# Kernel optimization log

Measured on AMD Instinct MI355X. Metric: run time of the kernel, lower is better.

## Reference

```python
import jax, jax.numpy as jnp
import numpy as np

B, L, IN, DM, DS, DC, EXP = 4, 1024, 256, 1024, 16, 4, 2
DI = EXP * DM            # d_inner = 2048
DTR = (DM + 15) // 16    # dt_rank = 64


def setup_inputs() -> dict:
    key = jax.random.key(0)
    ks = jax.random.split(key, 10)
    s = lambda k, sh, sc: jax.random.normal(k, sh, jnp.float32) * sc
    return {
        "x": s(ks[0], (B, L, IN), 1.0),
        "W_emb": s(ks[1], (DM, IN), IN ** -0.5),
        "b_emb": jnp.zeros((DM,), jnp.float32),
        "in_proj_w": s(ks[2], (2 * DI, DM), DM ** -0.5),
        "conv_w": s(ks[3], (DI, 1, DC), DC ** -0.5),
        "conv_b": jnp.zeros((DI,), jnp.float32),
        "x_proj_w": s(ks[4], (DTR + 2 * DS, DI), DI ** -0.5),
        "dt_proj_w": s(ks[5], (DI, DTR), DTR ** -0.5),
        "dt_proj_b": s(ks[6], (DI,), 0.1),
        "A_log": jnp.tile(jnp.log(jnp.arange(1, DS + 1, dtype=jnp.float32)), (DI, 1)),
        "D": jnp.ones((DI,), jnp.float32),
        "out_proj_w": s(ks[7], (DM, DI), DI ** -0.5),
        "fc_w": s(ks[8], (1, DM), DM ** -0.5),
        "fc_b": jnp.zeros((1,), jnp.float32),
    }


def _forward(x, W_emb, b_emb, in_proj_w, conv_w, conv_b, x_proj_w,
             dt_proj_w, dt_proj_b, A_log, D, out_proj_w, fc_w, fc_b):
    h = x @ W_emb.T + b_emb                      # [B,L,DM] input embedding
    xz = h @ in_proj_w.T                         # [B,L,2*DI]
    u, z = jnp.split(xz, 2, axis=-1)             # each [B,L,DI]
    # causal depthwise conv over time (pad left d_conv-1)
    uc = jax.lax.conv_general_dilated(
        u.transpose(0, 2, 1), conv_w, (1,), [(DC - 1, 0)],
        dimension_numbers=('NCH', 'OIH', 'NCH'), feature_group_count=DI)
    u = jax.nn.silu(uc.transpose(0, 2, 1) + conv_b)   # [B,L,DI]
    xdbl = u @ x_proj_w.T                        # [B,L,DTR+2*DS]
    dt, Bm, Cm = jnp.split(xdbl, [DTR, DTR + DS], axis=-1)
    delta = jax.nn.softplus(dt @ dt_proj_w.T + dt_proj_b)  # [B,L,DI]
    A = -jnp.exp(A_log)                          # [DI,DS]

    def step(hst, ins):
        d_t, B_t, C_t, u_t = ins                 # [B,DI],[B,DS],[B,DS],[B,DI]
        dA = jnp.exp(d_t[..., None] * A)         # [B,DI,DS]
        hst = dA * hst + (d_t * u_t)[..., None] * B_t[:, None, :]
        y = jnp.einsum('bds,bs->bd', hst, C_t)
        return hst, y

    h0 = jnp.zeros((B, DI, DS), u.dtype)
    _, ys = jax.lax.scan(step, h0, (delta.transpose(1, 0, 2),
                                    Bm.transpose(1, 0, 2),
                                    Cm.transpose(1, 0, 2),
                                    u.transpose(1, 0, 2)))
    y = ys.transpose(1, 0, 2) + D * u            # [B,L,DI] with D skip
    y = y * jax.nn.silu(z)                       # gate
    out = y @ out_proj_w.T                       # [B,L,DM]
    return out[:, -1, :] @ fc_w.T + fc_b         # [B,1]


def reference(x, W_emb, b_emb, in_proj_w, conv_w, conv_b, x_proj_w,
              dt_proj_w, dt_proj_b, A_log, D, out_proj_w, fc_w, fc_b):
    return _forward(x, W_emb, b_emb, in_proj_w, conv_w, conv_b, x_proj_w,
                    dt_proj_w, dt_proj_b, A_log, D, out_proj_w, fc_w, fc_b)
```

## Files before the change

### kernel.cpp

```cpp
#include <hip/hip_runtime.h>
#include <cstddef>
#include <cstdint>

namespace {

typedef _Float16 half8 __attribute__((ext_vector_type(8)));
typedef _Float16 half4 __attribute__((ext_vector_type(4)));
typedef float f32x4 __attribute__((ext_vector_type(4)));

constexpr int Bn   = 4;
constexpr int Ln   = 1024;
constexpr int INn  = 256;
constexpr int DMn  = 1024;
constexpr int DSn  = 16;
constexpr int DCn  = 4;
constexpr int DIn  = 2048;
constexpr int DTRn = 64;
constexpr int XPW  = DTRn + DSn;
constexpr int NCHUNK = 64;
constexpr int CHUNK  = Ln / NCHUNK;
constexpr int WCH  = 32;
constexpr int ML   = Bn * Ln;

__device__ __forceinline__ float silu_(float x) { return x / (1.f + __expf(-x)); }
__device__ __forceinline__ float softplus_(float x) {
    return fmaxf(x, 0.f) + __logf(1.f + __expf(-fabsf(x)));
}

__global__ __launch_bounds__(256)
void prep_mega(const float* __restrict__ x, _Float16* __restrict__ xh,
               const float* __restrict__ ip, _Float16* __restrict__ iph,
               const float* __restrict__ dtw, _Float16* __restrict__ dtwh,
               const float* __restrict__ W_emb, _Float16* __restrict__ W_embT,
               const float* __restrict__ x_proj, _Float16* __restrict__ xp_h,
               const float* __restrict__ fc_w, const float* __restrict__ out_w,
               float* __restrict__ wp,
               const float* __restrict__ b_emb, float* __restrict__ badd,
               const float* __restrict__ fc_b, float* __restrict__ out) {
    __shared__ float tile[32][33];
    const int bid = blockIdx.x, tid = threadIdx.x;
    if (bid < 4096) {
        const int n = bid;
        const float4 v = ((const float4*)ip)[n * 256 + tid];
        ((half4*)iph)[n * 256 + tid] =
            half4{(_Float16)v.x, (_Float16)v.y, (_Float16)v.z, (_Float16)v.w};
        const float4 bv = ((const float4*)b_emb)[tid];
        float s = v.x * bv.x + v.y * bv.y + v.z * bv.z + v.w * bv.w;
        for (int off = 32; off > 0; off >>= 1) s += __shfl_down(s, off);
        if ((tid & 63) == 0) tile[0][tid >> 6] = s;
        __syncthreads();
        if (tid == 0) badd[n] = tile[0][0] + tile[0][1] + tile[0][2] + tile[0][3];
    } else if (bid < 5248) {
        const float* in; _Float16* outp; int i;
        if (bid < 5120) { in = x;   outp = xh;   i = (bid - 4096) * 256 + tid; }
        else            { in = dtw; outp = dtwh; i = (bid - 5120) * 256 + tid; }
        const float4 v = ((const float4*)in)[i];
        ((half4*)outp)[i] = half4{(_Float16)v.x, (_Float16)v.y, (_Float16)v.z, (_Float16)v.w};
    } else if (bid < 5504) {
        const int bx = bid - 5248;
        const int m0 = (bx & 31) * 32, c0 = (bx >> 5) * 32;
        const int lc = tid & 31, lr = tid >> 5;
        #pragma unroll
        for (int ph = 0; ph < 4; ++ph)
            tile[lr + ph * 8][lc] = W_emb[(size_t)(m0 + lr + ph * 8) * INn + c0 + lc];
        __syncthreads();
        #pragma unroll
        for (int ph = 0; ph < 4; ++ph)
            W_embT[(size_t)(c0 + lr + ph * 8) * DMn + m0 + lc] = (_Float16)tile[lc][lr + ph * 8];
    } else if (bid < 5760) {
        const int i = (bid - 5504) * 256 + tid;
        const int r = i >> 9;
        const int c4 = i & 511;
        half4 h;
        if (r < XPW) {
            const float4 v = ((const float4*)(x_proj + (size_t)r * DIn))[c4];
            h = half4{(_Float16)v.x, (_Float16)v.y, (_Float16)v.z, (_Float16)v.w};
        } else {
            h = half4{(_Float16)0.f, (_Float16)0.f, (_Float16)0.f, (_Float16)0.f};
        }
        ((half4*)(xp_h + (size_t)r * DIn))[c4] = h;
    } else if (bid < 6016) {
        const int bx = bid - 5760;
        const int d = (bx & 7) * 256 + tid;
        const int c = bx >> 3;
        const int mstep = DMn / WCH;
        float s = 0.f;
        for (int m = c * mstep; m < (c + 1) * mstep; ++m)
            s += fc_w[m] * out_w[(size_t)m * DIn + d];
        wp[(size_t)c * DIn + d] = s;
    } else {
        if (tid < Bn) out[tid] = fc_b[0];
    }
}

__global__ __launch_bounds__(256)
void skgemm2(const _Float16* __restrict__ A, int lda,
             const _Float16* __restrict__ Bw, int ldb,
             float* __restrict__ P, int N, int Kc) {
    __shared__ _Float16 As[128 * 32];
    __shared__ _Float16 Bs[128 * 32];
    const int tid  = threadIdx.x;
    const int lane = tid & 63, wid = tid >> 6;
    const int wm = wid >> 1, wn = wid & 1;
    const int sk = blockIdx.x;
    const int m0 = blockIdx.y * 128;
    const int n0 = blockIdx.z * 128;
    const int M  = gridDim.y * 128;

    f32x4 acc[4][4] = {};
    const int kbeg = sk * Kc;
    for (int k0 = kbeg; k0 < kbeg + Kc; k0 += 32) {
        #pragma unroll
        for (int i = 0; i < 2; ++i) {
            const int off = tid * 16 + i * 4096;
            const int row = off >> 6;
            const int ch  = (off & 63) >> 1;
            const _Float16* ga = A  + (size_t)(m0 + row) * lda + k0 + ch;
            const _Float16* gb = Bw + (size_t)(n0 + row) * ldb + k0 + ch;
            __builtin_amdgcn_global_load_lds(
                (const __attribute__((address_space(1))) void*)ga,
                (__attribute__((address_space(3))) void*)(&As[off >> 1]), 16, 0, 0);
            __builtin_amdgcn_global_load_lds(
                (const __attribute__((address_space(1))) void*)gb,
                (__attribute__((address_space(3))) void*)(&Bs[off >> 1]), 16, 0, 0);
        }
        __syncthreads();
        const int ar = lane & 15;
        const int kq = (lane >> 4) * 8;
        half8 af[4], bf[4];
        #pragma unroll
        for (int i = 0; i < 4; ++i)
            af[i] = *(const half8*)&As[(wm * 64 + i * 16 + ar) * 32 + kq];
        #pragma unroll
        for (int j = 0; j < 4; ++j)
            bf[j] = *(const half8*)&Bs[(wn * 64 + j * 16 + ar) * 32 + kq];
        #pragma unroll
        for (int i = 0; i < 4; ++i)
            #pragma unroll
            for (int j = 0; j < 4; ++j)
                acc[i][j] = __builtin_amdgcn_mfma_f32_16x16x32_f16(af[i], bf[j], acc[i][j], 0, 0, 0);
        __syncthreads();
    }

    const int cr = (lane >> 4) * 4;
    const int cn = lane & 15;
    #pragma unroll
    for (int i = 0; i < 4; ++i) {
        #pragma unroll
        for (int j = 0; j < 4; ++j) {
            const int n = n0 + wn * 64 + j * 16 + cn;
            if (n < N) {
                #pragma unroll
                for (int r = 0; r < 4; ++r) {
                    const int m = m0 + wm * 64 + i * 16 + cr + r;
                    P[((size_t)sk * M + m) * N + n] = acc[i][j][r];
                }
            }
        }
    }
}

__global__ __launch_bounds__(256)
void skcomb(const float* __restrict__ P, _Float16* __restrict__ out, int total, int nsk) {
    const int i = blockIdx.x * 256 + threadIdx.x;
    if (i >= total) return;
    float s = 0.f;
    for (int k = 0; k < nsk; ++k) s += P[(size_t)k * total + i];
    out[i] = (_Float16)s;
}

__global__ __launch_bounds__(256)
void skcombB_clast(const float* __restrict__ P, _Float16* __restrict__ dtBh,
                   const _Float16* __restrict__ u, const float* __restrict__ x_proj,
                   float* __restrict__ Clast) {
    const int bid = blockIdx.x, tid = threadIdx.x;
    if (bid < 1280) {
        const int i = bid * 256 + tid;
        float s = 0.f;
        #pragma unroll
        for (int k = 0; k < 8; ++k) s += P[(size_t)k * (ML * XPW) + i];
        dtBh[i] = (_Float16)s;
    } else {
        const int wave = tid >> 6, lane = tid & 63;
        const int task = (bid - 1280) * 4 + wave;
        const int s_idx = task & 15, b = task >> 4;
        const _Float16* ur = u + ((size_t)b * Ln + (Ln - 1)) * DIn;
        const float* w = x_proj + (size_t)(XPW + s_idx) * DIn;
        float s = 0.f;
        for (int k = lane; k < DIn; k += 64) s += (float)ur[k] * w[k];
        for (int off = 32; off > 0; off >>= 1) s += __shfl_down(s, off);
        if (lane == 0) Clast[b * DSn + s_idx] = s;
    }
}

template<int ACT, bool HAS_BIAS>
__global__ __launch_bounds__(256)
void hgemm(const _Float16* __restrict__ A, int lda,
           const _Float16* __restrict__ Bw, int ldb,
           const float* __restrict__ bias,
           _Float16* __restrict__ Ch, int ldc,
           int N, int K) {
    __shared__ _Float16 As[128 * 32];
    __shared__ _Float16 Bs[128 * 32];
    const int tid  = threadIdx.x;
    const int lane = tid & 63, wid = tid >> 6;
    const int wm = wid >> 1, wn = wid & 1;
    const int m0 = blockIdx.y * 128, n0 = blockIdx.x * 128;

    f32x4 acc[4][4] = {};

    for (int k0 = 0; k0 < K; k0 += 32) {
        #pragma unroll
        for (int i = 0; i < 2; ++i) {
            const int off = tid * 16 + i * 4096;
            const int row = off >> 6;
            const int ch  = (off & 63) >> 1;
            const _Float16* ga = A  + (size_t)(m0 + row) * lda + k0 + ch;
            const _Float16* gb = Bw + (size_t)(n0 + row) * ldb + k0 + ch;
            __builtin_amdgcn_global_load_lds(
                (const __attribute__((address_space(1))) void*)ga,
                (__attribute__((address_space(3))) void*)(&As[off >> 1]), 16, 0, 0);
            __builtin_amdgcn_global_load_lds(
                (const __attribute__((address_space(1))) void*)gb,
                (__attribute__((address_space(3))) void*)(&Bs[off >> 1]), 16, 0, 0);
        }
        __syncthreads();

        const int ar = lane & 15;
        const int kq = (lane >> 4) * 8;
        half8 af[4], bf[4];
        #pragma unroll
        for (int i = 0; i < 4; ++i)
            af[i] = *(const half8*)&As[(wm * 64 + i * 16 + ar) * 32 + kq];
        #pragma unroll
        for (int j = 0; j < 4; ++j)
            bf[j] = *(const half8*)&Bs[(wn * 64 + j * 16 + ar) * 32 + kq];
        #pragma unroll
        for (int i = 0; i < 4; ++i)
            #pragma unroll
            for (int j = 0; j < 4; ++j)
                acc[i][j] = __builtin_amdgcn_mfma_f32_16x16x32_f16(af[i], bf[j], acc[i][j], 0, 0, 0);
        __syncthreads();
    }

    const int cr = (lane >> 4) * 4;
    const int cn = lane & 15;
    #pragma unroll
    for (int i = 0; i < 4; ++i) {
        #pragma unroll
        for (int j = 0; j < 4; ++j) {
            const int n = n0 + wn * 64 + j * 16 + cn;
            if (n < N) {
                #pragma unroll
                for (int r = 0; r < 4; ++r) {
                    const int m = m0 + wm * 64 + i * 16 + cr + r;
                    float v = acc[i][j][r];
                    if (HAS_BIAS) v += bias[n];
                    if (ACT == 1) v = softplus_(v);
                    Ch[(size_t)m * ldc + n] = (_Float16)v;
                }
            }
        }
    }
}

__global__ __launch_bounds__(256)
void conv_zlast(const _Float16* __restrict__ upre, const float* __restrict__ cw,
                const float* __restrict__ cb, _Float16* __restrict__ uh,
                const float* __restrict__ x, const _Float16* __restrict__ Wfh,
                const float* __restrict__ badd, float* __restrict__ zlast) {
    const int tid = threadIdx.x;
    const int bid = blockIdx.x;
    if (bid < 1024) {
        const int b  = bid >> 8;
        const int t0 = (bid & 255) * 4;
        const int d0 = tid * 8;
        const size_t rowbase = ((size_t)b * Ln + t0) * DIn + d0;

        half8 hzero;
        #pragma unroll
        for (int q = 0; q < 8; ++q) hzero[q] = (_Float16)0.f;

        half8 rows[7];
        if (t0 >= 3) {
            #pragma unroll
            for (int r = 0; r < 7; ++r)
                rows[r] = *(const half8*)(upre + rowbase + (ptrdiff_t)(r - 3) * DIn);
        } else {
            #pragma unroll
            for (int r = 0; r < 7; ++r) {
                const int t = t0 - 3 + r;
                rows[r] = (t >= 0) ? *(const half8*)(upre + rowbase + (ptrdiff_t)(r - 3) * DIn) : hzero;
            }
        }

        f32x4 cwq[8];
        float cbv[8];
        #pragma unroll
        for (int q = 0; q < 8; ++q) {
            cwq[q] = *(const f32x4*)(cw + (size_t)(d0 + q) * DCn);
            cbv[q] = cb[d0 + q];
        }

        #pragma unroll
        for (int s = 0; s < 4; ++s) {
            half8 o;
            #pragma unroll
            for (int q = 0; q < 8; ++q) {
                float acc = cbv[q];
                #pragma unroll
                for (int j = 0; j < DCn; ++j) acc += (float)rows[s + j][q] * cwq[q][j];
                o[q] = (_Float16)silu_(acc);
            }
            *(half8*)(uh + rowbase + (size_t)s * DIn) = o;
        }
    } else {
        const int task = (bid - 1024) * 256 + tid;
        const int j = task & (DIn - 1), b = task >> 11;
        const float4* x4 = (const float4*)(x + ((size_t)b * Ln + (Ln - 1)) * INn);
        const half4* w4 = (const half4*)(Wfh + (size_t)(DIn + j) * INn);
        float s = 0.f;
        #pragma unroll 8
        for (int q = 0; q < 64; ++q) {
            const float4 xv = x4[q];
            const half4 wv = w4[q];
            s += (float)wv[0] * xv.x + (float)wv[1] * xv.y
               + (float)wv[2] * xv.z + (float)wv[3] * xv.w;
        }
        zlast[(size_t)b * DIn + j] = s + badd[DIn + j];
    }
}

__global__ __launch_bounds__(256)
void scan_chunk_kernel(const _Float16* __restrict__ delta, const _Float16* __restrict__ u,
                       const _Float16* __restrict__ dtBh, const float* __restrict__ A_log,
                       float* __restrict__ cS, _Float16* __restrict__ cH) {
    const int d = blockIdx.x * 256 + threadIdx.x;
    const int c = blockIdx.y, b = blockIdx.z;
    float A[DSn], h[DSn];
    const float4* al = (const float4*)(A_log + (size_t)d * DSn);
    #pragma unroll
    for (int q = 0; q < 4; ++q) {
        const float4 v = al[q];
        A[q * 4 + 0] = -__expf(v.x); A[q * 4 + 1] = -__expf(v.y);
        A[q * 4 + 2] = -__expf(v.z); A[q * 4 + 3] = -__expf(v.w);
        h[q * 4 + 0] = 0.f; h[q * 4 + 1] = 0.f; h[q * 4 + 2] = 0.f; h[q * 4 + 3] = 0.f;
    }
    const float A0 = A[0];
    bool structured = true;
    #pragma unroll
    for (int s = 1; s < DSn; ++s)
        structured = structured && (fabsf(A[s] - (float)(s + 1) * A0) <= 1e-4f * (s + 1));

    float Ssum = 0.f;
    const size_t base = ((size_t)b * Ln + (size_t)c * CHUNK) * DIn + d;
    const _Float16* Bp = dtBh + ((size_t)b * Ln + (size_t)c * CHUNK) * XPW + DTRn;
    if (structured) {
        #pragma unroll 4
        for (int tt = 0; tt < CHUNK; ++tt) {
            const float dl = (float)delta[base + (size_t)tt * DIn];
            const float uu = (float)u[base + (size_t)tt * DIn];
            const float du = dl * uu;
            Ssum += dl;
            const half8 bv0 = *(const half8*)(Bp + tt * XPW);
            const half8 bv1 = *(const half8*)(Bp + tt * XPW + 8);
            float Bv[DSn];
            #pragma unroll
            for (int q = 0; q < 8; ++q) { Bv[q] = (float)bv0[q]; Bv[8 + q] = (float)bv1[q]; }
            const float e1 = __expf(dl * A0);
            const float e2 = e1 * e1, e4 = e2 * e2, e8 = e4 * e4;
            float E[DSn];
            E[0] = e1;      E[1] = e2;      E[2] = e2 * e1;  E[3] = e4;
            E[4] = e4 * e1; E[5] = e4 * e2; E[6] = E[5] * e1; E[7] = e8;
            E[8] = e8 * e1; E[9] = e8 * e2; E[10] = E[9] * e1; E[11] = e8 * e4;
            E[12] = E[11] * e1; E[13] = E[11] * e2; E[14] = E[13] * e1; E[15] = e8 * e8;
            #pragma unroll
            for (int s = 0; s < DSn; ++s) h[s] = E[s] * h[s] + du * Bv[s];
        }
    } else {
        #pragma unroll 4
        for (int tt = 0; tt < CHUNK; ++tt) {
            const float dl = (float)delta[base + (size_t)tt * DIn];
            const float uu = (float)u[base + (size_t)tt * DIn];
            const float du = dl * uu;
            Ssum += dl;
            const half8 bv0 = *(const half8*)(Bp + tt * XPW);
            const half8 bv1 = *(const half8*)(Bp + tt * XPW + 8);
            float Bv[DSn];
            #pragma unroll
            for (int q = 0; q < 8; ++q) { Bv[q] = (float)bv0[q]; Bv[8 + q] = (float)bv1[q]; }
            #pragma unroll
            for (int s = 0; s < DSn; ++s) h[s] = __expf(dl * A[s]) * h[s] + du * Bv[s];
        }
    }
    const size_t cidx = ((size_t)b * NCHUNK + c) * DIn + d;
    cS[cidx] = Ssum;
    half8 o0, o1;
    #pragma unroll
    for (int q = 0; q < 8; ++q) { o0[q] = (_Float16)h[q]; o1[q] = (_Float16)h[8 + q]; }
    *(half8*)(cH + cidx * DSn) = o0;
    *(half8*)(cH + cidx * DSn + 8) = o1;
}

__global__ __launch_bounds__(256)
void combine_v3(const float* __restrict__ cS, const _Float16* __restrict__ cH,
                const float* __restrict__ A_log, const float* __restrict__ Clast,
                const float* __restrict__ Dp, const _Float16* __restrict__ u,
                const float* __restrict__ zlast, const float* __restrict__ wp,
                float* __restrict__ out) {
    __shared__ float acc[16];
    const int tid = threadIdx.x;
    const int s = tid & 15;
    const int d = blockIdx.x * 16 + (tid >> 4);
    const int b = blockIdx.y;
    const float A = -__expf(A_log[(size_t)d * DSn + s]);
    float h = 0.f;
    const size_t cb0 = (size_t)b * NCHUNK;
    for (int c = 0; c < NCHUNK; ++c) {
        const size_t cidx = (cb0 + c) * DIn + d;
        h = __expf(A * cS[cidx]) * h + (float)cH[cidx * DSn + s];
    }
    float y = h * Clast[b * DSn + s];
    y += __shfl_xor(y, 1);
    y += __shfl_xor(y, 2);
    y += __shfl_xor(y, 4);
    y += __shfl_xor(y, 8);
    if (s == 0) {
        const float ul = (float)u[((size_t)b * Ln + (Ln - 1)) * DIn + d];
        float yy = y + Dp[d] * ul;
        yy *= silu_(zlast[(size_t)b * DIn + d]);
        float w = 0.f;
        #pragma unroll
        for (int c = 0; c < WCH; ++c) w += wp[(size_t)c * DIn + d];
        acc[tid >> 4] = yy * w;
    }
    __syncthreads();
    if (tid == 0) {
        float t = 0.f;
        #pragma unroll
        for (int i = 0; i < 16; ++i) t += acc[i];
        atomicAdd(&out[b], t);
    }
}

}

extern "C" void kernel_launch(void* const* d_in, const int* in_sizes, int n_in,
                              void* d_out, int out_size, void* d_ws, size_t ws_size,
                              hipStream_t stream) {
    (void)in_sizes; (void)n_in; (void)out_size; (void)ws_size;
    const float* x       = (const float*)d_in[0];
    const float* W_emb   = (const float*)d_in[1];
    const float* b_emb   = (const float*)d_in[2];
    const float* in_proj = (const float*)d_in[3];
    const float* conv_w  = (const float*)d_in[4];
    const float* conv_b  = (const float*)d_in[5];
    const float* x_proj  = (const float*)d_in[6];
    const float* dt_w    = (const float*)d_in[7];
    const float* dt_b    = (const float*)d_in[8];
    const float* A_log   = (const float*)d_in[9];
    const float* Dp      = (const float*)d_in[10];
    const float* out_w   = (const float*)d_in[11];
    const float* fc_w    = (const float*)d_in[12];
    const float* fc_b    = (const float*)d_in[13];
    float* out = (float*)d_out;
    char* w8 = (char*)d_ws;

    const size_t MB = 1ull << 20;
    _Float16* upreh    = (_Float16*)(w8);
    _Float16* uh       = (_Float16*)(w8 + 16 * MB);
    float*    wfoldP   = (float*)(w8 + 32 * MB);
    _Float16* deltah   = (_Float16*)(w8 + 32 * MB);
    float*    skp      = (float*)(w8 + 48 * MB);
    float*    cS       = skp;
    _Float16* cH       = (_Float16*)(w8 + 50 * MB);
    _Float16* dtBh     = (_Float16*)(w8 + 67 * MB);
    _Float16* xh       = (_Float16*)(w8 + 68 * MB);
    _Float16* W_embT_h = (_Float16*)(w8 + 70 * MB);
    _Float16* in_projh = (_Float16*)(w8 + 71 * MB);
    _Float16* xp_h     = (_Float16*)(w8 + 79 * MB);
    _Float16* dt_wh    = (_Float16*)(w8 + 80 * MB);
    _Float16* Wfoldh   = (_Float16*)(w8 + 81 * MB);
    float*    wp       = (float*)(w8 + 83 * MB);
    float*    badd     = (float*)(w8 + 84 * MB);
    float*    zlast    = badd + 4096;
    float*    Clast    = zlast + (size_t)Bn * DIn;

    prep_mega<<<6017, 256, 0, stream>>>(x, xh, in_proj, in_projh, dt_w, dt_wh,
                                        W_emb, W_embT_h, x_proj, xp_h,
                                        fc_w, out_w, wp, b_emb, badd, fc_b, out);

    skgemm2<<<dim3(4, ML / 128, 2), 256, 0, stream>>>(
        in_projh, DMn, W_embT_h, DMn, wfoldP, INn, 256);
    skcomb<<<(ML * INn + 255) / 256, 256, 0, stream>>>(wfoldP, Wfoldh, ML * INn, 4);

    hgemm<0, true><<<dim3(DIn / 128, ML / 128), 256, 0, stream>>>(
        xh, INn, Wfoldh, INn, badd, upreh, DIn, DIn, INn);
    conv_zlast<<<1056, 256, 0, stream>>>(upreh, conv_w, conv_b, uh, x, Wfoldh, badd, zlast);
    skgemm2<<<dim3(8, ML / 128, 1), 256, 0, stream>>>(uh, DIn, xp_h, DIn, skp, XPW, 256);
    skcombB_clast<<<1296, 256, 0, stream>>>(skp, dtBh, uh, x_proj, Clast);
    hgemm<1, true><<<dim3(DIn / 128, ML / 128), 256, 0, stream>>>(
        dtBh, XPW, dt_wh, DTRn, dt_b, deltah, DIn, DIn, DTRn);
    scan_chunk_kernel<<<dim3(DIn / 256, NCHUNK, Bn), 256, 0, stream>>>(
        deltah, uh, dtBh, A_log, cS, cH);
    combine_v3<<<dim3(DIn / 16, Bn), 256, 0, stream>>>(
        cS, cH, A_log, Clast, Dp, uh, zlast, wp, out);
}
```

Measured before the change: 127.4 us.

## Fuse all stages into a persistent cooperative kernel with grid-wide syncs

Replaces the chain of separate kernel launches with one persistent cooperative kernel. It loops over each phase's tasks and separates the phases with grid.sync(), and falls back to the separate kernels if the cooperative launch fails. The aim is to remove per-launch overhead and the gaps between dependent kernels. In exchange the grid is capped at 512 blocks of 256 threads, which can lower parallelism in the large phases, and each grid barrier has its own cost.

```diff
diff --git a/kernel.cpp b/kernel.cpp
--- a/kernel.cpp
+++ b/kernel.cpp
@@ -1,6 +1,9 @@
 #include <hip/hip_runtime.h>
+#include <hip/hip_cooperative_groups.h>
 #include <cstddef>
 #include <cstdint>
+
+namespace cg = cooperative_groups;
 
 namespace {
 
@@ -22,118 +25,67 @@
 constexpr int WCH  = 32;
 constexpr int ML   = Bn * Ln;
 
+constexpr int T_PREP = 6017;
+constexpr int T_WFOLD = 256;
+constexpr int T_WFSUM = ML * INn / 4 / 256;
+constexpr int T_UPRE = 512;
+constexpr int T_CONVZ = 1056;
+constexpr int T_DTB = 256;
+constexpr int T_DTBSUM = 1296;
+constexpr int T_DELTA = 512;
+constexpr int T_SCAN = 2048;
+constexpr int T_COMB = 512;
+
 __device__ __forceinline__ float silu_(float x) { return x / (1.f + __expf(-x)); }
 __device__ __forceinline__ float softplus_(float x) {
     return fmaxf(x, 0.f) + __logf(1.f + __expf(-fabsf(x)));
 }
 
-__global__ __launch_bounds__(256)
-void prep_mega(const float* __restrict__ x, _Float16* __restrict__ xh,
-               const float* __restrict__ ip, _Float16* __restrict__ iph,
-               const float* __restrict__ dtw, _Float16* __restrict__ dtwh,
-               const float* __restrict__ W_emb, _Float16* __restrict__ W_embT,
-               const float* __restrict__ x_proj, _Float16* __restrict__ xp_h,
-               const float* __restrict__ fc_w, const float* __restrict__ out_w,
-               float* __restrict__ wp,
-               const float* __restrict__ b_emb, float* __restrict__ badd,
-               const float* __restrict__ fc_b, float* __restrict__ out) {
-    __shared__ float tile[32][33];
-    const int bid = blockIdx.x, tid = threadIdx.x;
-    if (bid < 4096) {
-        const int n = bid;
-        const float4 v = ((const float4*)ip)[n * 256 + tid];
-        ((half4*)iph)[n * 256 + tid] =
-            half4{(_Float16)v.x, (_Float16)v.y, (_Float16)v.z, (_Float16)v.w};
-        const float4 bv = ((const float4*)b_emb)[tid];
-        float s = v.x * bv.x + v.y * bv.y + v.z * bv.z + v.w * bv.w;
-        for (int off = 32; off > 0; off >>= 1) s += __shfl_down(s, off);
-        if ((tid & 63) == 0) tile[0][tid >> 6] = s;
-        __syncthreads();
-        if (tid == 0) badd[n] = tile[0][0] + tile[0][1] + tile[0][2] + tile[0][3];
-    } else if (bid < 5248) {
-        const float* in; _Float16* outp; int i;
-        if (bid < 5120) { in = x;   outp = xh;   i = (bid - 4096) * 256 + tid; }
-        else            { in = dtw; outp = dtwh; i = (bid - 5120) * 256 + tid; }
-        const float4 v = ((const float4*)in)[i];
-        ((half4*)outp)[i] = half4{(_Float16)v.x, (_Float16)v.y, (_Float16)v.z, (_Float16)v.w};
-    } else if (bid < 5504) {
-        const int bx = bid - 5248;
-        const int m0 = (bx & 31) * 32, c0 = (bx >> 5) * 32;
-        const int lc = tid & 31, lr = tid >> 5;
-        #pragma unroll
-        for (int ph = 0; ph < 4; ++ph)
-            tile[lr + ph * 8][lc] = W_emb[(size_t)(m0 + lr + ph * 8) * INn + c0 + lc];
-        __syncthreads();
-        #pragma unroll
-        for (int ph = 0; ph < 4; ++ph)
-            W_embT[(size_t)(c0 + lr + ph * 8) * DMn + m0 + lc] = (_Float16)tile[lc][lr + ph * 8];
-    } else if (bid < 5760) {
-        const int i = (bid - 5504) * 256 + tid;
-        const int r = i >> 9;
-        const int c4 = i & 511;
-        half4 h;
-        if (r < XPW) {
-            const float4 v = ((const float4*)(x_proj + (size_t)r * DIn))[c4];
-            h = half4{(_Float16)v.x, (_Float16)v.y, (_Float16)v.z, (_Float16)v.w};
-        } else {
-            h = half4{(_Float16)0.f, (_Float16)0.f, (_Float16)0.f, (_Float16)0.f};
-        }
-        ((half4*)(xp_h + (size_t)r * DIn))[c4] = h;
-    } else if (bid < 6016) {
-        const int bx = bid - 5760;
-        const int d = (bx & 7) * 256 + tid;
-        const int c = bx >> 3;
-        const int mstep = DMn / WCH;
-        float s = 0.f;
-        for (int m = c * mstep; m < (c + 1) * mstep; ++m)
-            s += fc_w[m] * out_w[(size_t)m * DIn + d];
-        wp[(size_t)c * DIn + d] = s;
-    } else {
-        if (tid < Bn) out[tid] = fc_b[0];
-    }
-}
-
-__global__ __launch_bounds__(256)
-void skgemm2(const _Float16* __restrict__ A, int lda,
-             const _Float16* __restrict__ Bw, int ldb,
-             float* __restrict__ P, int N, int Kc) {
-    __shared__ _Float16 As[128 * 32];
-    __shared__ _Float16 Bs[128 * 32];
-    const int tid  = threadIdx.x;
-    const int lane = tid & 63, wid = tid >> 6;
+struct MegaP {
+    const float *x, *b_emb, *in_proj, *conv_w, *conv_b, *x_proj, *dt_b, *A_log, *Dp,
+                *out_w, *fc_w, *fc_b, *W_emb, *dt_w;
+    float* out;
+    _Float16 *xh, *iph, *dtwh, *W_embT, *xp_h, *upreh, *uh, *deltah, *dtBh, *Wfoldh;
+    float *wfoldP, *skp, *cS;
+    _Float16 *cH;
+    float *wp, *badd, *zlast, *Clast;
+};
+
+template<int EPI>
+__device__ __forceinline__ void gemm_tile(
+    const _Float16* __restrict__ A, int lda,
+    const _Float16* __restrict__ Bw, int ldb,
+    int m0, int n0, int kbeg, int kend, int N,
+    float* __restrict__ Pout,
+    _Float16* __restrict__ Ch, int ldc,
+    const float* __restrict__ bias,
+    _Float16* As, _Float16* Bs, int tid)
+{
+    const int lane = tid & 63;
+    const int wid  = tid >> 6;
     const int wm = wid >> 1, wn = wid & 1;
-    const int sk = blockIdx.x;
-    const int m0 = blockIdx.y * 128;
-    const int n0 = blockIdx.z * 128;
-    const int M  = gridDim.y * 128;
-
     f32x4 acc[4][4] = {};
-    const int kbeg = sk * Kc;
-    for (int k0 = kbeg; k0 < kbeg + Kc; k0 += 32) {
+    for (int k0 = kbeg; k0 < kend; k0 += 32) {
         #pragma unroll
         for (int i = 0; i < 2; ++i) {
             const int off = tid * 16 + i * 4096;
             const int row = off >> 6;
             const int ch  = (off & 63) >> 1;
-            const _Float16* ga = A  + (size_t)(m0 + row) * lda + k0 + ch;
-            const _Float16* gb = Bw + (size_t)(n0 + row) * ldb + k0 + ch;
             __builtin_amdgcn_global_load_lds(
-                (const __attribute__((address_space(1))) void*)ga,
-                (__attribute__((address_space(3))) void*)(&As[off >> 1]), 16, 0, 0);
+                (const __attribute__((address_space(1))) void*)(A + (size_t)(m0 + row) * lda + k0 + ch),
+                (__attribute__((address_space(3))) void*)(As + (off >> 1)), 16, 0, 0);
             __builtin_amdgcn_global_load_lds(
-                (const __attribute__((address_space(1))) void*)gb,
-                (__attribute__((address_space(3))) void*)(&Bs[off >> 1]), 16, 0, 0);
+                (const __attribute__((address_space(1))) void*)(Bw + (size_t)(n0 + row) * ldb + k0 + ch),
+                (__attribute__((address_space(3))) void*)(Bs + (off >> 1)), 16, 0, 0);
         }
         __syncthreads();
         const int ar = lane & 15;
         const int kq = (lane >> 4) * 8;
         half8 af[4], bf[4];
         #pragma unroll
-        for (int i = 0; i < 4; ++i)
-            af[i] = *(const half8*)&As[(wm * 64 + i * 16 + ar) * 32 + kq];
-        #pragma unroll
-        for (int j = 0; j < 4; ++j)
-            bf[j] = *(const half8*)&Bs[(wn * 64 + j * 16 + ar) * 32 + kq];
+        for (int i = 0; i < 4; ++i) af[i] = *(const half8*)(As + (wm * 64 + i * 16 + ar) * 32 + kq);
+        #pragma unroll
+        for (int j = 0; j < 4; ++j) bf[j] = *(const half8*)(Bs + (wn * 64 + j * 16 + ar) * 32 + kq);
         #pragma unroll
         for (int i = 0; i < 4; ++i)
             #pragma unroll
@@ -141,11 +93,10 @@
                 acc[i][j] = __builtin_amdgcn_mfma_f32_16x16x32_f16(af[i], bf[j], acc[i][j], 0, 0, 0);
         __syncthreads();
     }
-
     const int cr = (lane >> 4) * 4;
     const int cn = lane & 15;
     #pragma unroll
-    for (int i = 0; i < 4; ++i) {
+    for (int i = 0; i < 4; ++i)
         #pragma unroll
         for (int j = 0; j < 4; ++j) {
             const int n = n0 + wn * 64 + j * 16 + cn;
@@ -153,155 +104,128 @@
                 #pragma unroll
                 for (int r = 0; r < 4; ++r) {
                     const int m = m0 + wm * 64 + i * 16 + cr + r;
-                    P[((size_t)sk * M + m) * N + n] = acc[i][j][r];
+                    if (EPI == 0) {
+                        Pout[(size_t)m * N + n] = acc[i][j][r];
+                    } else {
+                        float v = acc[i][j][r] + bias[n];
+                        if (EPI == 2) v = softplus_(v);
+                        Ch[(size_t)m * ldc + n] = (_Float16)v;
+                    }
                 }
             }
         }
-    }
-}
-
-__global__ __launch_bounds__(256)
-void skcomb(const float* __restrict__ P, _Float16* __restrict__ out, int total, int nsk) {
-    const int i = blockIdx.x * 256 + threadIdx.x;
-    if (i >= total) return;
-    float s = 0.f;
-    for (int k = 0; k < nsk; ++k) s += P[(size_t)k * total + i];
-    out[i] = (_Float16)s;
-}
-
-__global__ __launch_bounds__(256)
-void skcombB_clast(const float* __restrict__ P, _Float16* __restrict__ dtBh,
-                   const _Float16* __restrict__ u, const float* __restrict__ x_proj,
-                   float* __restrict__ Clast) {
-    const int bid = blockIdx.x, tid = threadIdx.x;
-    if (bid < 1280) {
-        const int i = bid * 256 + tid;
+}
+
+__device__ __forceinline__ void ph_prep(const MegaP& p, int task, int tid, float* shf) {
+    if (task < 4096) {
+        const int n = task;
+        const float4 v = ((const float4*)p.in_proj)[n * 256 + tid];
+        ((half4*)p.iph)[n * 256 + tid] =
+            half4{(_Float16)v.x, (_Float16)v.y, (_Float16)v.z, (_Float16)v.w};
+        const float4 bv = ((const float4*)p.b_emb)[tid];
+        float s = v.x * bv.x + v.y * bv.y + v.z * bv.z + v.w * bv.w;
+        for (int off = 32; off > 0; off >>= 1) s += __shfl_down(s, off);
+        if ((tid & 63) == 0) shf[tid >> 6] = s;
+        __syncthreads();
+        if (tid == 0) p.badd[n] = shf[0] + shf[1] + shf[2] + shf[3];
+    } else if (task < 5248) {
+        const float* in; _Float16* outp; int i;
+        if (task < 5120) { in = p.x;    outp = p.xh;   i = (task - 4096) * 256 + tid; }
+        else             { in = p.dt_w; outp = p.dtwh; i = (task - 5120) * 256 + tid; }
+        const float4 v = ((const float4*)in)[i];
+        ((half4*)outp)[i] = half4{(_Float16)v.x, (_Float16)v.y, (_Float16)v.z, (_Float16)v.w};
+    } else if (task < 5504) {
+        const int bx = task - 5248;
+        const int m0 = (bx & 31) * 32, c0 = (bx >> 5) * 32;
+        const int lc = tid & 31, lr = tid >> 5;
+        float (*tile)[33] = (float(*)[33])(void*)shf;
+        #pragma unroll
+        for (int ph = 0; ph < 4; ++ph)
+            tile[lr + ph * 8][lc] = p.W_emb[(size_t)(m0 + lr + ph * 8) * INn + c0 + lc];
+        __syncthreads();
+        #pragma unroll
+        for (int ph = 0; ph < 4; ++ph)
+            p.W_embT[(size_t)(c0 + lr + ph * 8) * DMn + m0 + lc] = (_Float16)tile[lc][lr + ph * 8];
+    } else if (task < 5760) {
+        const int i = (task - 5504) * 256 + tid;
+        const int r = i >> 9;
+        const int c4 = i & 511;
+        half4 h;
+        if (r < XPW) {
+            const float4 v = ((const float4*)(p.x_proj + (size_t)r * DIn))[c4];
+            h = half4{(_Float16)v.x, (_Float16)v.y, (_Float16)v.z, (_Float16)v.w};
+        } else {
+            h = half4{(_Float16)0.f, (_Float16)0.f, (_Float16)0.f, (_Float16)0.f};
+        }
+        ((half4*)(p.xp_h + (size_t)r * DIn))[c4] = h;
+    } else if (task < 6016) {
+        const int bx = task - 5760;
+        const int d = (bx & 7) * 256 + tid;
+        const int c = bx >> 3;
+        const int mstep = DMn / WCH;
         float s = 0.f;
-        #pragma unroll
-        for (int k = 0; k < 8; ++k) s += P[(size_t)k * (ML * XPW) + i];
-        dtBh[i] = (_Float16)s;
+        for (int m = c * mstep; m < (c + 1) * mstep; ++m)
+            s += p.fc_w[m] * p.out_w[(size_t)m * DIn + d];
+        p.wp[(size_t)c * DIn + d] = s;
     } else {
-        const int wave = tid >> 6, lane = tid & 63;
-        const int task = (bid - 1280) * 4 + wave;
-        const int s_idx = task & 15, b = task >> 4;
-        const _Float16* ur = u + ((size_t)b * Ln + (Ln - 1)) * DIn;
-        const float* w = x_proj + (size_t)(XPW + s_idx) * DIn;
-        float s = 0.f;
-        for (int k = lane; k < DIn; k += 64) s += (float)ur[k] * w[k];
-        for (int off = 32; off > 0; off >>= 1) s += __shfl_down(s, off);
-        if (lane == 0) Clast[b * DSn + s_idx] = s;
-    }
-}
-
-template<int ACT, bool HAS_BIAS>
-__global__ __launch_bounds__(256)
-void hgemm(const _Float16* __restrict__ A, int lda,
-           const _Float16* __restrict__ Bw, int ldb,
-           const float* __restrict__ bias,
-           _Float16* __restrict__ Ch, int ldc,
-           int N, int K) {
-    __shared__ _Float16 As[128 * 32];
-    __shared__ _Float16 Bs[128 * 32];
-    const int tid  = threadIdx.x;
-    const int lane = tid & 63, wid = tid >> 6;
-    const int wm = wid >> 1, wn = wid & 1;
-    const int m0 = blockIdx.y * 128, n0 = blockIdx.x * 128;
-
-    f32x4 acc[4][4] = {};
-
-    for (int k0 = 0; k0 < K; k0 += 32) {
-        #pragma unroll
-        for (int i = 0; i < 2; ++i) {
-            const int off = tid * 16 + i * 4096;
-            const int row = off >> 6;
-            const int ch  = (off & 63) >> 1;
-            const _Float16* ga = A  + (size_t)(m0 + row) * lda + k0 + ch;
-            const _Float16* gb = Bw + (size_t)(n0 + row) * ldb + k0 + ch;
-            __builtin_amdgcn_global_load_lds(
-                (const __attribute__((address_space(1))) void*)ga,
-                (__attribute__((address_space(3))) void*)(&As[off >> 1]), 16, 0, 0);
-            __builtin_amdgcn_global_load_lds(
-                (const __attribute__((address_space(1))) void*)gb,
-                (__attribute__((address_space(3))) void*)(&Bs[off >> 1]), 16, 0, 0);
-        }
-        __syncthreads();
-
-        const int ar = lane & 15;
-        const int kq = (lane >> 4) * 8;
-        half8 af[4], bf[4];
-        #pragma unroll
-        for (int i = 0; i < 4; ++i)
-            af[i] = *(const half8*)&As[(wm * 64 + i * 16 + ar) * 32 + kq];
-        #pragma unroll
-        for (int j = 0; j < 4; ++j)
-            bf[j] = *(const half8*)&Bs[(wn * 64 + j * 16 + ar) * 32 + kq];
-        #pragma unroll
-        for (int i = 0; i < 4; ++i)
-            #pragma unroll
-            for (int j = 0; j < 4; ++j)
-                acc[i][j] = __builtin_amdgcn_mfma_f32_16x16x32_f16(af[i], bf[j], acc[i][j], 0, 0, 0);
-        __syncthreads();
-    }
-
-    const int cr = (lane >> 4) * 4;
-    const int cn = lane & 15;
+        if (tid < Bn) p.out[tid] = p.fc_b[0];
+    }
+}
+
+__device__ __forceinline__ void ph_wfold(const MegaP& p, int task, int tid,
+                                         _Float16* As, _Float16* Bs) {
+    const int sk = task >> 6;
+    const int mt = (task & 63) >> 1;
+    const int nt = task & 1;
+    gemm_tile<0>(p.iph, DMn, p.W_embT, DMn, mt * 128, nt * 128,
+                 sk * 256, sk * 256 + 256, INn,
+                 p.wfoldP + (size_t)sk * ML * INn, nullptr, 0, nullptr, As, Bs, tid);
+}
+
+__device__ __forceinline__ void ph_wfoldsum(const MegaP& p, int i) {
+    float4 s = ((const float4*)p.wfoldP)[i];
     #pragma unroll
-    for (int i = 0; i < 4; ++i) {
-        #pragma unroll
-        for (int j = 0; j < 4; ++j) {
-            const int n = n0 + wn * 64 + j * 16 + cn;
-            if (n < N) {
-                #pragma unroll
-                for (int r = 0; r < 4; ++r) {
-                    const int m = m0 + wm * 64 + i * 16 + cr + r;
-                    float v = acc[i][j][r];
-                    if (HAS_BIAS) v += bias[n];
-                    if (ACT == 1) v = softplus_(v);
-                    Ch[(size_t)m * ldc + n] = (_Float16)v;
-                }
-            }
-        }
-    }
-}
-
-__global__ __launch_bounds__(256)
-void conv_zlast(const _Float16* __restrict__ upre, const float* __restrict__ cw,
-                const float* __restrict__ cb, _Float16* __restrict__ uh,
-                const float* __restrict__ x, const _Float16* __restrict__ Wfh,
-                const float* __restrict__ badd, float* __restrict__ zlast) {
-    const int tid = threadIdx.x;
-    const int bid = blockIdx.x;
-    if (bid < 1024) {
-        const int b  = bid >> 8;
-        const int t0 = (bid & 255) * 4;
+    for (int k = 1; k < 4; ++k) {
+        const float4 v = ((const float4*)(p.wfoldP + (size_t)k * ML * INn))[i];
+        s.x += v.x; s.y += v.y; s.z += v.z; s.w += v.w;
+    }
+    ((half4*)p.Wfoldh)[i] = half4{(_Float16)s.x, (_Float16)s.y, (_Float16)s.z, (_Float16)s.w};
+}
+
+__device__ __forceinline__ void ph_upre(const MegaP& p, int task, int tid,
+                                        _Float16* As, _Float16* Bs) {
+    gemm_tile<1>(p.xh, INn, p.Wfoldh, INn, (task >> 4) * 128, (task & 15) * 128,
+                 0, 256, DIn, nullptr, p.upreh, DIn, p.badd, As, Bs, tid);
+}
+
+__device__ __forceinline__ void ph_convz(const MegaP& p, int task, int tid) {
+    if (task < 1024) {
+        const int b  = task >> 8;
+        const int t0 = (task & 255) * 4;
         const int d0 = tid * 8;
         const size_t rowbase = ((size_t)b * Ln + t0) * DIn + d0;
-
         half8 hzero;
         #pragma unroll
         for (int q = 0; q < 8; ++q) hzero[q] = (_Float16)0.f;
-
         half8 rows[7];
         if (t0 >= 3) {
             #pragma unroll
             for (int r = 0; r < 7; ++r)
-                rows[r] = *(const half8*)(upre + rowbase + (ptrdiff_t)(r - 3) * DIn);
+                rows[r] = *(const half8*)(p.upreh + rowbase + (ptrdiff_t)(r - 3) * DIn);
         } else {
             #pragma unroll
             for (int r = 0; r < 7; ++r) {
                 const int t = t0 - 3 + r;
-                rows[r] = (t >= 0) ? *(const half8*)(upre + rowbase + (ptrdiff_t)(r - 3) * DIn) : hzero;
+                rows[r] = (t >= 0) ? *(const half8*)(p.upreh + rowbase + (ptrdiff_t)(r - 3) * DIn) : hzero;
             }
         }
-
         f32x4 cwq[8];
         float cbv[8];
         #pragma unroll
         for (int q = 0; q < 8; ++q) {
-            cwq[q] = *(const f32x4*)(cw + (size_t)(d0 + q) * DCn);
-            cbv[q] = cb[d0 + q];
-        }
-
+            cwq[q] = *(const f32x4*)(p.conv_w + (size_t)(d0 + q) * DCn);
+            cbv[q] = p.conv_b[d0 + q];
+        }
         #pragma unroll
         for (int s = 0; s < 4; ++s) {
             half8 o;
@@ -312,13 +236,13 @@
                 for (int j = 0; j < DCn; ++j) acc += (float)rows[s + j][q] * cwq[q][j];
                 o[q] = (_Float16)silu_(acc);
             }
-            *(half8*)(uh + rowbase + (size_t)s * DIn) = o;
+            *(half8*)(p.uh + rowbase + (size_t)s * DIn) = o;
         }
     } else {
-        const int task = (bid - 1024) * 256 + tid;
-        const int j = task & (DIn - 1), b = task >> 11;
-        const float4* x4 = (const float4*)(x + ((size_t)b * Ln + (Ln - 1)) * INn);
-        const half4* w4 = (const half4*)(Wfh + (size_t)(DIn + j) * INn);
+        const int t = (task - 1024) * 256 + tid;
+        const int j = t & (DIn - 1), b = t >> 11;
+        const float4* x4 = (const float4*)(p.x + ((size_t)b * Ln + (Ln - 1)) * INn);
+        const half4* w4 = (const half4*)(p.Wfoldh + (size_t)(DIn + j) * INn);
         float s = 0.f;
         #pragma unroll 8
         for (int q = 0; q < 64; ++q) {
@@ -327,18 +251,52 @@
             s += (float)wv[0] * xv.x + (float)wv[1] * xv.y
                + (float)wv[2] * xv.z + (float)wv[3] * xv.w;
         }
-        zlast[(size_t)b * DIn + j] = s + badd[DIn + j];
-    }
-}
-
-__global__ __launch_bounds__(256)
-void scan_chunk_kernel(const _Float16* __restrict__ delta, const _Float16* __restrict__ u,
-                       const _Float16* __restrict__ dtBh, const float* __restrict__ A_log,
-                       float* __restrict__ cS, _Float16* __restrict__ cH) {
-    const int d = blockIdx.x * 256 + threadIdx.x;
-    const int c = blockIdx.y, b = blockIdx.z;
+        p.zlast[(size_t)b * DIn + j] = s + p.badd[DIn + j];
+    }
+}
+
+__device__ __forceinline__ void ph_dtb(const MegaP& p, int task, int tid,
+                                       _Float16* As, _Float16* Bs) {
+    const int sk = task >> 5;
+    const int mt = task & 31;
+    gemm_tile<0>(p.uh, DIn, p.xp_h, DIn, mt * 128, 0,
+                 sk * 256, sk * 256 + 256, XPW,
+                 p.skp + (size_t)sk * ML * XPW, nullptr, 0, nullptr, As, Bs, tid);
+}
+
+__device__ __forceinline__ void ph_dtbsum(const MegaP& p, int task, int tid) {
+    if (task < 1280) {
+        const int i = task * 256 + tid;
+        float s = 0.f;
+        #pragma unroll
+        for (int k = 0; k < 8; ++k) s += p.skp[(size_t)k * (ML * XPW) + i];
+        p.dtBh[i] = (_Float16)s;
+    } else {
+        const int wave = tid >> 6, lane = tid & 63;
+        const int t = (task - 1280) * 4 + wave;
+        const int s_idx = t & 15, b = t >> 4;
+        const _Float16* ur = p.uh + ((size_t)b * Ln + (Ln - 1)) * DIn;
+        const float* w = p.x_proj + (size_t)(XPW + s_idx) * DIn;
+        float s = 0.f;
+        for (int k = lane; k < DIn; k += 64) s += (float)ur[k] * w[k];
+        for (int off = 32; off > 0; off >>= 1) s += __shfl_down(s, off);
+        if (lane == 0) p.Clast[b * DSn + s_idx] = s;
+    }
+}
+
+__device__ __forceinline__ void ph_delta(const MegaP& p, int task, int tid,
+                                         _Float16* As, _Float16* Bs) {
+    gemm_tile<2>(p.dtBh, XPW, p.dtwh, DTRn, (task >> 4) * 128, (task & 15) * 128,
+                 0, 64, DIn, nullptr, p.deltah, DIn, p.dt_b, As, Bs, tid);
+}
+
+__device__ __forceinline__ void ph_scan(const MegaP& p, int task, int tid) {
+    const int dgrp = task & 7;
+    const int c = (task >> 3) & 63;
+    const int b = task >> 9;
+    const int d = dgrp * 256 + tid;
     float A[DSn], h[DSn];
-    const float4* al = (const float4*)(A_log + (size_t)d * DSn);
+    const float4* al = (const float4*)(p.A_log + (size_t)d * DSn);
     #pragma unroll
     for (int q = 0; q < 4; ++q) {
         const float4 v = al[q];
@@ -351,15 +309,14 @@
     #pragma unroll
     for (int s = 1; s < DSn; ++s)
         structured = structured && (fabsf(A[s] - (float)(s + 1) * A0) <= 1e-4f * (s + 1));
-
     float Ssum = 0.f;
     const size_t base = ((size_t)b * Ln + (size_t)c * CHUNK) * DIn + d;
-    const _Float16* Bp = dtBh + ((size_t)b * Ln + (size_t)c * CHUNK) * XPW + DTRn;
+    const _Float16* Bp = p.dtBh + ((size_t)b * Ln + (size_t)c * CHUNK) * XPW + DTRn;
     if (structured) {
         #pragma unroll 4
         for (int tt = 0; tt < CHUNK; ++tt) {
-            const float dl = (float)delta[base + (size_t)tt * DIn];
-            const float uu = (float)u[base + (size_t)tt * DIn];
+            const float dl = (float)p.deltah[base + (size_t)tt * DIn];
+            const float uu = (float)p.uh[base + (size_t)tt * DIn];
             const float du = dl * uu;
             Ssum += dl;
             const half8 bv0 = *(const half8*)(Bp + tt * XPW);
@@ -380,8 +337,8 @@
     } else {
         #pragma unroll 4
         for (int tt = 0; tt < CHUNK; ++tt) {
-            const float dl = (float)delta[base + (size_t)tt * DIn];
-            const float uu = (float)u[base + (size_t)tt * DIn];
+            const float dl = (float)p.deltah[base + (size_t)tt * DIn];
+            const float uu = (float)p.uh[base + (size_t)tt * DIn];
             const float du = dl * uu;
             Ssum += dl;
             const half8 bv0 = *(const half8*)(Bp + tt * XPW);
@@ -394,53 +351,115 @@
         }
     }
     const size_t cidx = ((size_t)b * NCHUNK + c) * DIn + d;
-    cS[cidx] = Ssum;
+    p.cS[cidx] = Ssum;
     half8 o0, o1;
     #pragma unroll
     for (int q = 0; q < 8; ++q) { o0[q] = (_Float16)h[q]; o1[q] = (_Float16)h[8 + q]; }
-    *(half8*)(cH + cidx * DSn) = o0;
-    *(half8*)(cH + cidx * DSn + 8) = o1;
-}
-
-__global__ __launch_bounds__(256)
-void combine_v3(const float* __restrict__ cS, const _Float16* __restrict__ cH,
-                const float* __restrict__ A_log, const float* __restrict__ Clast,
-                const float* __restrict__ Dp, const _Float16* __restrict__ u,
-                const float* __restrict__ zlast, const float* __restrict__ wp,
-                float* __restrict__ out) {
-    __shared__ float acc[16];
-    const int tid = threadIdx.x;
+    *(half8*)(p.cH + cidx * DSn) = o0;
+    *(half8*)(p.cH + cidx * DSn + 8) = o1;
+}
+
+__device__ __forceinline__ void ph_combine(const MegaP& p, int task, int tid, float* accs) {
+    const int dgrp = task & 127;
+    const int b = task >> 7;
     const int s = tid & 15;
-    const int d = blockIdx.x * 16 + (tid >> 4);
-    const int b = blockIdx.y;
-    const float A = -__expf(A_log[(size_t)d * DSn + s]);
+    const int d = dgrp * 16 + (tid >> 4);
+    const float A = -__expf(p.A_log[(size_t)d * DSn + s]);
     float h = 0.f;
     const size_t cb0 = (size_t)b * NCHUNK;
     for (int c = 0; c < NCHUNK; ++c) {
         const size_t cidx = (cb0 + c) * DIn + d;
-        h = __expf(A * cS[cidx]) * h + (float)cH[cidx * DSn + s];
-    }
-    float y = h * Clast[b * DSn + s];
+        h = __expf(A * p.cS[cidx]) * h + (float)p.cH[cidx * DSn + s];
+    }
+    float y = h * p.Clast[b * DSn + s];
     y += __shfl_xor(y, 1);
     y += __shfl_xor(y, 2);
     y += __shfl_xor(y, 4);
     y += __shfl_xor(y, 8);
     if (s == 0) {
-        const float ul = (float)u[((size_t)b * Ln + (Ln - 1)) * DIn + d];
-        float yy = y + Dp[d] * ul;
-        yy *= silu_(zlast[(size_t)b * DIn + d]);
+        const float ul = (float)p.uh[((size_t)b * Ln + (Ln - 1)) * DIn + d];
+        float yy = y + p.Dp[d] * ul;
+        yy *= silu_(p.zlast[(size_t)b * DIn + d]);
         float w = 0.f;
         #pragma unroll
-        for (int c = 0; c < WCH; ++c) w += wp[(size_t)c * DIn + d];
-        acc[tid >> 4] = yy * w;
+        for (int c = 0; c < WCH; ++c) w += p.wp[(size_t)c * DIn + d];
+        accs[tid >> 4] = yy * w;
     }
     __syncthreads();
     if (tid == 0) {
         float t = 0.f;
         #pragma unroll
-        for (int i = 0; i < 16; ++i) t += acc[i];
-        atomicAdd(&out[b], t);
-    }
+        for (int i = 0; i < 16; ++i) t += accs[i];
+        atomicAdd(&p.out[b], t);
+    }
+}
+
+__global__ __launch_bounds__(256, 2)
+void mamba_mega(MegaP p) {
+    __shared__ _Float16 As[128 * 32];
+    __shared__ _Float16 Bs[128 * 32];
+    const int tid = threadIdx.x;
+    const int bid = blockIdx.x;
+    const int nb  = gridDim.x;
+    cg::grid_group grid = cg::this_grid();
+
+    for (int t = bid; t < T_PREP; t += nb) { ph_prep(p, t, tid, (float*)As); __syncthreads(); }
+    grid.sync();
+    for (int t = bid; t < T_WFOLD; t += nb) ph_wfold(p, t, tid, As, Bs);
+    grid.sync();
+    for (int i = bid * 256 + tid; i < ML * INn / 4; i += nb * 256) ph_wfoldsum(p, i);
+    grid.sync();
+    for (int t = bid; t < T_UPRE; t += nb) ph_upre(p, t, tid, As, Bs);
+    grid.sync();
+    for (int t = bid; t < T_CONVZ; t += nb) ph_convz(p, t, tid);
+    grid.sync();
+    for (int t = bid; t < T_DTB; t += nb) ph_dtb(p, t, tid, As, Bs);
+    grid.sync();
+    for (int t = bid; t < T_DTBSUM; t += nb) ph_dtbsum(p, t, tid);
+    grid.sync();
+    for (int t = bid; t < T_DELTA; t += nb) ph_delta(p, t, tid, As, Bs);
+    grid.sync();
+    for (int t = bid; t < T_SCAN; t += nb) ph_scan(p, t, tid);
+    grid.sync();
+    for (int t = bid; t < T_COMB; t += nb) { ph_combine(p, t, tid, (float*)Bs); __syncthreads(); }
+}
+
+__global__ __launch_bounds__(256) void k_prep(MegaP p) {
+    __shared__ float shf[32 * 33];
+    ph_prep(p, blockIdx.x, threadIdx.x, shf);
+}
+__global__ __launch_bounds__(256) void k_wfold(MegaP p) {
+    __shared__ _Float16 As[128 * 32]; __shared__ _Float16 Bs[128 * 32];
+    ph_wfold(p, blockIdx.x, threadIdx.x, As, Bs);
+}
+__global__ __launch_bounds__(256) void k_wfoldsum(MegaP p) {
+    const int i = blockIdx.x * 256 + threadIdx.x;
+    if (i < ML * INn / 4) ph_wfoldsum(p, i);
+}
+__global__ __launch_bounds__(256) void k_upre(MegaP p) {
+    __shared__ _Float16 As[128 * 32]; __shared__ _Float16 Bs[128 * 32];
+    ph_upre(p, blockIdx.x, threadIdx.x, As, Bs);
+}
+__global__ __launch_bounds__(256) void k_convz(MegaP p) {
+    ph_convz(p, blockIdx.x, threadIdx.x);
+}
+__global__ __launch_bounds__(256) void k_dtb(MegaP p) {
+    __shared__ _Float16 As[128 * 32]; __shared__ _Float16 Bs[128 * 32];
+    ph_dtb(p, blockIdx.x, threadIdx.x, As, Bs);
+}
+__global__ __launch_bounds__(256) void k_dtbsum(MegaP p) {
+    ph_dtbsum(p, blockIdx.x, threadIdx.x);
+}
+__global__ __launch_bounds__(256) void k_delta(MegaP p) {
+    __shared__ _Float16 As[128 * 32]; __shared__ _Float16 Bs[128 * 32];
+    ph_delta(p, blockIdx.x, threadIdx.x, As, Bs);
+}
+__global__ __launch_bounds__(256) void k_scan(MegaP p) {
+    ph_scan(p, blockIdx.x, threadIdx.x);
+}
+__global__ __launch_bounds__(256) void k_combine(MegaP p) {
+    __shared__ float accs[16];
+    ph_combine(p, blockIdx.x, threadIdx.x, accs);
 }
 
 }
@@ -486,23 +505,36 @@
     float*    zlast    = badd + 4096;
     float*    Clast    = zlast + (size_t)Bn * DIn;
 
-    prep_mega<<<6017, 256, 0, stream>>>(x, xh, in_proj, in_projh, dt_w, dt_wh,
-                                        W_emb, W_embT_h, x_proj, xp_h,
-                                        fc_w, out_w, wp, b_emb, badd, fc_b, out);
-
-    skgemm2<<<dim3(4, ML / 128, 2), 256, 0, stream>>>(
-        in_projh, DMn, W_embT_h, DMn, wfoldP, INn, 256);
-    skcomb<<<(ML * INn + 255) / 256, 256, 0, stream>>>(wfoldP, Wfoldh, ML * INn, 4);
-
-    hgemm<0, true><<<dim3(DIn / 128, ML / 128), 256, 0, stream>>>(
-        xh, INn, Wfoldh, INn, badd, upreh, DIn, DIn, INn);
-    conv_zlast<<<1056, 256, 0, stream>>>(upreh, conv_w, conv_b, uh, x, Wfoldh, badd, zlast);
-    skgemm2<<<dim3(8, ML / 128, 1), 256, 0, stream>>>(uh, DIn, xp_h, DIn, skp, XPW, 256);
-    skcombB_clast<<<1296, 256, 0, stream>>>(skp, dtBh, uh, x_proj, Clast);
-    hgemm<1, true><<<dim3(DIn / 128, ML / 128), 256, 0, stream>>>(
-        dtBh, XPW, dt_wh, DTRn, dt_b, deltah, DIn, DIn, DTRn);
-    scan_chunk_kernel<<<dim3(DIn / 256, NCHUNK, Bn), 256, 0, stream>>>(
-        deltah, uh, dtBh, A_log, cS, cH);
-    combine_v3<<<dim3(DIn / 16, Bn), 256, 0, stream>>>(
-        cS, cH, A_log, Clast, Dp, uh, zlast, wp, out);
-}
+    MegaP p;
+    p.x = x; p.b_emb = b_emb; p.in_proj = in_proj; p.conv_w = conv_w; p.conv_b = conv_b;
+    p.x_proj = x_proj; p.dt_b = dt_b; p.A_log = A_log; p.Dp = Dp; p.out_w = out_w;
+    p.fc_w = fc_w; p.fc_b = fc_b; p.W_emb = W_emb; p.dt_w = dt_w;
+    p.out = out;
+    p.xh = xh; p.iph = in_projh; p.dtwh = dt_wh; p.W_embT = W_embT_h; p.xp_h = xp_h;
+    p.upreh = upreh; p.uh = uh; p.deltah = deltah; p.dtBh = dtBh; p.Wfoldh = Wfoldh;
+    p.wfoldP = wfoldP; p.skp = skp; p.cS = cS; p.cH = cH;
+    p.wp = wp; p.badd = badd; p.zlast = zlast; p.Clast = Clast;
+
+    bool coop_ok = false;
+    int occ = 0;
+    if (hipOccupancyMaxActiveBlocksPerMultiprocessor(&occ, mamba_mega, 256, 0) == hipSuccess
+        && occ >= 1) {
+        int nb = occ * 256;
+        if (nb > 512) nb = 512;
+        void* args[] = { &p };
+        coop_ok = (hipLaunchCooperativeKernel((void*)mamba_mega, dim3(nb), dim3(256),
+                                              args, 0, stream) == hipSuccess);
+    }
+    if (!coop_ok) {
+        k_prep    <<<T_PREP,   256, 0, stream>>>(p);
+        k_wfold   <<<T_WFOLD,  256, 0, stream>>>(p);
+        k_wfoldsum<<<T_WFSUM,  256, 0, stream>>>(p);
+        k_upre    <<<T_UPRE,   256, 0, stream>>>(p);
+        k_convz   <<<T_CONVZ,  256, 0, stream>>>(p);
+        k_dtb     <<<T_DTB,    256, 0, stream>>>(p);
+        k_dtbsum  <<<T_DTBSUM, 256, 0, stream>>>(p);
+        k_delta   <<<T_DELTA,  256, 0, stream>>>(p);
+        k_scan    <<<T_SCAN,   256, 0, stream>>>(p);
+        k_combine <<<T_COMB,   256, 0, stream>>>(p);
+    }
+}
```

After: 429.5 us. 3.37x slower.
